# Optimization experiments

Measured on AMD Instinct MI355X. Metric: run time of the kernel, lower is better.

## Reference

```python
import jax, jax.numpy as jnp
import numpy as np

N = 8192
D_IN = 512
HID = 1024
EMB = 64
N_EFF = 2
N_CLASSES = 16
MARGIN = 0.01


def setup_inputs() -> dict:
    key = jax.random.key(0)
    ks = jax.random.split(key, 10)
    data = jax.random.normal(ks[0], (N, D_IN), dtype=jnp.float32)
    labels = jax.random.randint(ks[1], (N,), 0, N_CLASSES).astype(jnp.float32)
    x = jnp.concatenate([labels[:, None], data], axis=1)  # [N, 1+D_IN]

    def lin(k, fan_in, fan_out):
        return jax.random.normal(k, (fan_in, fan_out), dtype=jnp.float32) / np.sqrt(fan_in)

    return {
        "x": x,
        "W1": lin(ks[2], D_IN, HID), "b1": jnp.zeros((HID,), jnp.float32),
        "W2": lin(ks[3], HID, EMB), "b2": jnp.zeros((EMB,), jnp.float32),
        "W3": lin(ks[4], EMB, HID), "b3": jnp.zeros((HID,), jnp.float32),
        "W4": lin(ks[5], HID, D_IN), "b4": jnp.zeros((D_IN,), jnp.float32),
    }


def reference(x, W1, b1, W2, b2, W3, b3, W4, b4):
    labels = x[:, 0]
    data = x[:, 1:]

    # encoder / decoder (tanh MLP autoencoder)
    embedding = jnp.tanh(data @ W1 + b1) @ W2 + b2          # [N, EMB]
    decoded = jnp.tanh(embedding @ W3 + b3) @ W4 + b4       # [N, D_IN]

    conserved = embedding[:, N_EFF:]                        # [N, C]
    n_conserved = conserved.shape[1]

    # labels.expand + unique(return_inverse) on row-replicated labels is
    # equivalent to comparing the labels directly.
    lbl = labels.astype(jnp.int32)
    Y = lbl[:, None] != lbl[None, :]                        # [N, N] bool

    # D_mean[i,j] = mean_d (c_i - c_j)^2, via Gram-matrix algebra (one pass,
    # no [N,N,C] intermediate).
    sq = jnp.sum(conserved * conserved, axis=1)             # [N]
    gram = conserved @ conserved.T                          # [N, N]
    D_mean = jnp.maximum(sq[:, None] + sq[None, :] - 2.0 * gram, 0.0) / n_conserved

    Yf = Y.astype(D_mean.dtype)
    n_diff = jnp.sum(Yf)
    C_sim = jnp.sum(Yf * D_mean) / (n_diff + 1.0)
    C_diff = jnp.sum((1.0 - Yf) * jnp.maximum(0.0, MARGIN - D_mean)) / (
        (D_mean.shape[0] * D_mean.shape[1] - n_diff) + 1.0)

    return decoded, C_sim, C_diff
```

## Files before the change

### kernel.cpp

```cpp
#include <hip/hip_runtime.h>
#include <stdint.h>

#define NROWS 8192
#define DIN   512
#define HIDN  1024
#define EMBN  64
#define NCONS 62
#define NCLS  16
#define MARGINF 0.01f

typedef unsigned short u16;
typedef __attribute__((ext_vector_type(8))) short short8;
typedef __attribute__((ext_vector_type(4))) float floatx4;

__device__ __forceinline__ u16 f32_to_bf16(float f) {
  union { float f; uint32_t u; } x; x.f = f;
  uint32_t u = x.u;
  uint32_t r = (u + 0x7FFFu + ((u >> 16) & 1u)) >> 16;
  return (u16)r;
}

__device__ __forceinline__ float bf16_to_f32(u16 h) {
  union { uint32_t u; float f; } x; x.u = (uint32_t)h << 16;
  return x.f;
}

__device__ __forceinline__ float fast_tanh(float x) {
  float xc = fminf(fmaxf(x, -10.f), 10.f);
  float e = __expf(2.f * xc);
  return (e - 1.f) * __builtin_amdgcn_rcpf(e + 1.f);
}

__device__ __forceinline__ void load_lds16(const u16* g, u16* l) {
  __builtin_amdgcn_global_load_lds(
      (const __attribute__((address_space(1))) void*)g,
      (__attribute__((address_space(3))) void*)l, 16, 0, 0);
}

__device__ __forceinline__ void pack_tile(const float* __restrict__ W,
                                          u16* __restrict__ Wp,
                                          int N, int KU, int t, int lane)
{
  const int r = lane >> 2, slot = lane & 3;
  const int c = slot ^ ((r >> 1) & 3);
  const int nt = t / KU, ku = t - nt * KU;
  const int n = nt * 16 + r;
  const int kb = ku * 32 + c * 8;
  short8 v;
#pragma unroll
  for (int j = 0; j < 8; ++j) v[j] = (short)f32_to_bf16(W[(size_t)(kb + j) * N + n]);
  *(short8*)(Wp + ((size_t)t * 64 + lane) * 8) = v;
}

__global__ __launch_bounds__(256)
void prep_all(const float* __restrict__ x,
              const float* __restrict__ W1, const float* __restrict__ W2,
              const float* __restrict__ W3, const float* __restrict__ W4,
              u16* __restrict__ A0p, u16* __restrict__ W1p,
              u16* __restrict__ W2p, u16* __restrict__ W3p,
              u16* __restrict__ W4p, float* __restrict__ slab,
              int* __restrict__ labels, int* __restrict__ hist32)
{
  __shared__ int hh[NCLS];
  const int b = blockIdx.x;
  const int tid = threadIdx.x;
  const int tl = tid >> 6, lane = tid & 63;
  if (b < 2048) {
    if (b < 32) {
      if (tid < NCLS) hh[tid] = 0;
      const int row = b * 256 + tid;
      const int lab = (int)x[(size_t)row * 513];
      labels[row] = lab;
      __syncthreads();
      atomicAdd(&hh[lab], 1);
      __syncthreads();
      if (tid < NCLS) hist32[b * NCLS + tid] = hh[tid];
    }
    const int t = b * 4 + tl;
    const int rt = t >> 4, ku = t & 15;
    const int r = lane & 15, q = lane >> 4;
    const float* src = x + (size_t)(rt * 16 + r) * 513 + 1 + ku * 32 + q * 8;
    short8 v;
#pragma unroll
    for (int j = 0; j < 8; ++j) v[j] = (short)f32_to_bf16(src[j]);
    *(short8*)(A0p + ((size_t)t * 64 + lane) * 8) = v;
  } else if (b < 2304) {
    pack_tile(W1, W1p, 1024, 16, (b - 2048) * 4 + tl, lane);
  } else if (b < 2336) {
    pack_tile(W2, W2p, 64, 32, (b - 2304) * 4 + tl, lane);
  } else if (b < 2368) {
    pack_tile(W3, W3p, 1024, 2, (b - 2336) * 4 + tl, lane);
  } else if (b < 2624) {
    pack_tile(W4, W4p, 512, 32, (b - 2368) * 4 + tl, lane);
  } else {
    for (int i = tid; i < 4096; i += 256) slab[i] = 0.f;
  }
}

__global__ __launch_bounds__(256)
void gemm12(const u16* __restrict__ A0p, const u16* __restrict__ W1p,
            const float* __restrict__ b1, const u16* __restrict__ W2p,
            float* __restrict__ Ef4,
            const int* __restrict__ labels, const int* __restrict__ hist32,
            int* __restrict__ offs, int* __restrict__ counts,
            int* __restrict__ idx)
{
  __shared__ u16 lB[2][16 * 512];
  __shared__ u16 Hc[4][64 * 66];
  __shared__ int colsum[NCLS], preblk[NCLS], scur[NCLS];

  const int tid = threadIdx.x, wave = tid >> 6, lane = tid & 63;

  if (blockIdx.x >= 128) {
    const int sb = (blockIdx.x - 128) * 4 + blockIdx.y;
    if (tid < NCLS) {
      int s = 0, p = 0;
      for (int b2 = 0; b2 < 32; ++b2) {
        const int h = hist32[b2 * NCLS + tid];
        s += h;
        if (b2 < sb * 2) p += h;
      }
      colsum[tid] = s;
      preblk[tid] = p;
    }
    __syncthreads();
    if (tid < NCLS) {
      int o = 0;
      for (int c = 0; c < tid; ++c) o += colsum[c];
      scur[tid] = o + preblk[tid];
      if (sb == 0) {
        counts[tid] = colsum[tid];
        offs[tid] = o;
        if (tid == NCLS - 1) offs[NCLS] = o + colsum[NCLS - 1];
      }
    }
    __syncthreads();
    for (int i = tid; i < 512; i += 256) {
      const int row = sb * 512 + i;
      const int p = atomicAdd(&scur[labels[row]], 1);
      idx[p] = row;
    }
    return;
  }

  const int quad = lane >> 4, l15 = lane & 15;
  const int wm = wave >> 1, wn = wave & 1;
  const int xslot = (l15 >> 1) & 3;
  const int m0 = blockIdx.x * 64;
  const int g = blockIdx.y;

  floatx4 Hacc[4][2][2];
#pragma unroll
  for (int c = 0; c < 4; ++c)
#pragma unroll
    for (int i = 0; i < 2; ++i)
#pragma unroll
      for (int j = 0; j < 2; ++j) Hacc[c][i][j] = (floatx4){0.f, 0.f, 0.f, 0.f};

#pragma unroll
  for (int u = 0; u < 4; ++u) {
    const int jt = wave + u * 4;
    load_lds16(W1p + (size_t)((g * 16 + jt) * 16) * 512 + lane * 8, lB[0] + jt * 512);
  }
  __syncthreads();

  for (int s = 0; s < 16; ++s) {
    const int p = s & 1;
    if (s < 15) {
#pragma unroll
      for (int u = 0; u < 4; ++u) {
        const int jt = wave + u * 4;
        load_lds16(W1p + (size_t)((g * 16 + jt) * 16 + s + 1) * 512 + lane * 8,
                   lB[1 - p] + jt * 512);
      }
    }
    short8 af[2];
#pragma unroll
    for (int i = 0; i < 2; ++i)
      af[i] = *(const short8*)(A0p +
               (size_t)((blockIdx.x * 4 + wm * 2 + i) * 16 + s) * 512 + lane * 8);
#pragma unroll
    for (int c = 0; c < 4; ++c)
#pragma unroll
      for (int j = 0; j < 2; ++j) {
        const short8 bf = *(const short8*)(lB[p] + (c * 4 + wn * 2 + j) * 512
                              + l15 * 32 + ((quad ^ xslot) << 3));
#pragma unroll
        for (int i = 0; i < 2; ++i)
          Hacc[c][i][j] = __builtin_amdgcn_mfma_f32_16x16x32_bf16(af[i], bf, Hacc[c][i][j], 0, 0, 0);
      }
    __syncthreads();
  }

  u16* lW2 = &lB[0][0];
#pragma unroll
  for (int u = 0; u < 8; ++u) {
    const int t = wave * 8 + u;
    load_lds16(W2p + (size_t)((t >> 3) * 32 + g * 8 + (t & 7)) * 512 + lane * 8,
               lW2 + t * 512);
  }
#pragma unroll
  for (int c = 0; c < 4; ++c)
#pragma unroll
    for (int j = 0; j < 2; ++j) {
      const int col = wn * 32 + j * 16 + l15;
      const float bv = b1[g * 256 + c * 64 + col];
#pragma unroll
      for (int i = 0; i < 2; ++i)
#pragma unroll
        for (int r = 0; r < 4; ++r)
          Hc[c][(wm * 32 + i * 16 + quad * 4 + r) * 66 + col] =
              f32_to_bf16(fast_tanh(Hacc[c][i][j][r] + bv));
    }
  __syncthreads();

  floatx4 Eacc[2][2];
#pragma unroll
  for (int i = 0; i < 2; ++i)
#pragma unroll
    for (int j = 0; j < 2; ++j) Eacc[i][j] = (floatx4){0.f, 0.f, 0.f, 0.f};

#pragma unroll
  for (int es = 0; es < 8; ++es) {
    const int cc = es >> 1, hh2 = es & 1;
    short8 af2[2];
#pragma unroll
    for (int i = 0; i < 2; ++i)
      af2[i] = *(const short8*)(Hc[cc] + (wm * 32 + i * 16 + l15) * 66 + hh2 * 32 + quad * 8);
#pragma unroll
    for (int j = 0; j < 2; ++j) {
      const short8 bf = *(const short8*)(lW2 + ((wn * 2 + j) * 8 + es) * 512
                            + l15 * 32 + ((quad ^ xslot) << 3));
#pragma unroll
      for (int i = 0; i < 2; ++i)
        Eacc[i][j] = __builtin_amdgcn_mfma_f32_16x16x32_bf16(af2[i], bf, Eacc[i][j], 0, 0, 0);
    }
  }

  float* Efg = Ef4 + (size_t)g * NROWS * 64;
#pragma unroll
  for (int i = 0; i < 2; ++i)
#pragma unroll
    for (int j = 0; j < 2; ++j) {
      const int col = wn * 32 + j * 16 + l15;
#pragma unroll
      for (int r = 0; r < 4; ++r) {
        const int row = m0 + wm * 32 + i * 16 + quad * 4 + r;
        Efg[(size_t)row * 64 + col] = Eacc[i][j][r];
      }
    }
}

__global__ __launch_bounds__(256)
void gemm3(const u16* __restrict__ Ebf, const u16* __restrict__ W3p,
           const float* __restrict__ b3, u16* __restrict__ T)
{
  const int tid = threadIdx.x, wave = tid >> 6, lane = tid & 63;
  const int quad = lane >> 4, l15 = lane & 15;
  const int wm = wave >> 1, wn = wave & 1;
  const int c0 = blockIdx.x * 256;
  const int m0 = blockIdx.y * 64;
  const int lamb = l15 * 4 + (quad ^ ((l15 >> 1) & 3));

  floatx4 acc[2][8];
#pragma unroll
  for (int i = 0; i < 2; ++i)
#pragma unroll
    for (int jj = 0; jj < 8; ++jj) acc[i][jj] = (floatx4){0.f, 0.f, 0.f, 0.f};

#pragma unroll
  for (int kk = 0; kk < 2; ++kk) {
    short8 af[2];
#pragma unroll
    for (int i = 0; i < 2; ++i)
      af[i] = *(const short8*)(Ebf + (size_t)(m0 + wm * 32 + i * 16 + l15) * 64
                                   + kk * 32 + quad * 8);
#pragma unroll
    for (int jj = 0; jj < 8; ++jj) {
      const int nt = (c0 >> 4) + wn * 8 + jj;
      const short8 bf = *(const short8*)(W3p + (size_t)(nt * 2 + kk) * 512 + lamb * 8);
#pragma unroll
      for (int i = 0; i < 2; ++i)
        acc[i][jj] = __builtin_amdgcn_mfma_f32_16x16x32_bf16(af[i], bf, acc[i][jj], 0, 0, 0);
    }
  }

#pragma unroll
  for (int i = 0; i < 2; ++i)
#pragma unroll
    for (int jj = 0; jj < 8; ++jj) {
      const int col = c0 + wn * 128 + jj * 16 + l15;
      const float bv = b3[col];
#pragma unroll
      for (int r = 0; r < 4; ++r) {
        const int row = m0 + wm * 32 + i * 16 + quad * 4 + r;
        T[(size_t)row * 1024 + col] = f32_to_bf16(fast_tanh(acc[i][jj][r] + bv));
      }
    }
}

__global__ __launch_bounds__(256)
void gemm4(const u16* __restrict__ T, const u16* __restrict__ W4p,
           const float* __restrict__ b4, float* __restrict__ out)
{
  __shared__ u16 lA[2][16 * 512];
  __shared__ u16 lB[2][8 * 512];

  const int tid = threadIdx.x, wave = tid >> 6, lane = tid & 63;
  const int quad = lane >> 4, l15 = lane & 15;
  const int wm = wave >> 1, wn = wave & 1;
  const int xslot = (l15 >> 1) & 3;
  const int m0 = blockIdx.y * 128;
  const int n0 = blockIdx.x * 64;
  const int srow = lane >> 2;
  const int schunk = (lane & 3) ^ ((lane >> 3) & 3);

  auto stage = [&](int s, int buf) {
#pragma unroll
    for (int q = 0; q < 6; ++q) {
      const int u = wave + q * 4;
      if (u < 16) {
        const int rg = u >> 1, kh = u & 1;
        load_lds16(T + (size_t)(m0 + rg * 16 + srow) * 1024 + s * 64 + kh * 32 + schunk * 8,
                   (buf ? lA[1] : lA[0]) + u * 512 + lane * 8);
      } else {
        const int v = u - 16, nt = v >> 1, kh = v & 1;
        load_lds16(W4p + (size_t)(((n0 >> 4) + nt) * 32 + s * 2 + kh) * 512 + lane * 8,
                   (buf ? lB[1] : lB[0]) + v * 512 + lane * 8);
      }
    }
  };

  stage(0, 0);
  __syncthreads();

  floatx4 acc[4][2];
#pragma unroll
  for (int i = 0; i < 4; ++i)
#pragma unroll
    for (int j = 0; j < 2; ++j) acc[i][j] = (floatx4){0.f, 0.f, 0.f, 0.f};

  for (int s = 0; s < 16; ++s) {
    const int p = s & 1;
    if (s < 15) stage(s + 1, 1 - p);
#pragma unroll
    for (int kk = 0; kk < 2; ++kk) {
      short8 af[4], bf[2];
#pragma unroll
      for (int i = 0; i < 4; ++i)
        af[i] = *(const short8*)(lA[p] + ((wm * 4 + i) * 2 + kk) * 512
                                 + l15 * 32 + ((quad ^ xslot) << 3));
#pragma unroll
      for (int j = 0; j < 2; ++j)
        bf[j] = *(const short8*)(lB[p] + ((wn * 2 + j) * 2 + kk) * 512
                                 + l15 * 32 + ((quad ^ xslot) << 3));
#pragma unroll
      for (int i = 0; i < 4; ++i)
#pragma unroll
        for (int j = 0; j < 2; ++j)
          acc[i][j] = __builtin_amdgcn_mfma_f32_16x16x32_bf16(af[i], bf[j], acc[i][j], 0, 0, 0);
    }
    __syncthreads();
  }

#pragma unroll
  for (int i = 0; i < 4; ++i)
#pragma unroll
    for (int j = 0; j < 2; ++j) {
      const int col = n0 + wn * 32 + j * 16 + l15;
      const float bv = b4[col];
#pragma unroll
      for (int r = 0; r < 4; ++r) {
        const int row = m0 + wm * 64 + i * 16 + quad * 4 + r;
        out[(size_t)row * 512 + col] = acc[i][j][r] + bv;
      }
    }
}

__global__ __launch_bounds__(256)
void stats_sq(const float* __restrict__ Ef4, const float* __restrict__ b2,
              const int* __restrict__ labels, u16* __restrict__ Ebf,
              float* __restrict__ sqrow, float* __restrict__ vsum,
              float* __restrict__ Ssum)
{
  __shared__ float lv[NCLS][64];
  __shared__ float lsq[NCLS][64];
  const int tid = threadIdx.x;
  for (int i = tid; i < NCLS * 64; i += 256) {
    ((float*)lv)[i] = 0.f; ((float*)lsq)[i] = 0.f;
  }
  __syncthreads();

  const int wave = tid >> 6, lane = tid & 63;
  const float bv = b2[lane];
  const int base = blockIdx.x * 32 + wave * 8;
  for (int r = 0; r < 8; ++r) {
    const int row = base + r;
    const int c = labels[row];
    float acc = bv;
#pragma unroll
    for (int g = 0; g < 4; ++g)
      acc += Ef4[((size_t)g * NROWS + row) * 64 + lane];
    const u16 h = f32_to_bf16(acc);
    Ebf[(size_t)row * 64 + lane] = h;
    float v = bf16_to_f32(h);
    if (lane < 2) v = 0.f;
    const float v2 = v * v;
    atomicAdd(&lv[c][lane], v);
    atomicAdd(&lsq[c][lane], v2);
    float s = v2;
    for (int o = 32; o > 0; o >>= 1) s += __shfl_xor(s, o);
    if (lane == 0) sqrow[row] = s;
  }
  __syncthreads();

  for (int i = tid; i < NCLS * 64; i += 256) {
    const int c = i >> 6, k = i & 63;
    if (k >= 2) atomicAdd(&vsum[c * NCONS + k - 2], lv[c][k]);
  }
  if (tid < NCLS) {
    float s = 0.f;
    for (int k = 0; k < 64; ++k) s += lsq[tid][k];
    atomicAdd(&Ssum[tid], s);
  }
}

__global__ __launch_bounds__(256)
void pairwise_mfma(const u16* __restrict__ Ebf, const float* __restrict__ sqrow,
                   const int* __restrict__ idx, const int* __restrict__ offs,
                   float* __restrict__ pair_sum)
{
  const int cls = blockIdx.y;
  int p = blockIdx.x, ti = 0, cnt = 6;
  while (p >= cnt) { p -= cnt; ++ti; --cnt; }
  const int tj = ti + p;

  const int start = offs[cls];
  const int n = offs[cls + 1] - start;
  if (ti * 128 >= n || tj * 128 >= n) return;

  constexpr int LDA = 66;
  __shared__ u16 Li[128 * LDA];
  __shared__ u16 Lj[128 * LDA];
  __shared__ float sqI[128], sqJ[128];
  __shared__ float red4[4];

  const int tid = threadIdx.x;
  for (int e = tid; e < 2048; e += 256) {
    const int t = e >> 10;
    const int row = (e >> 3) & 127;
    const int ch = e & 7;
    const int g = (t ? tj : ti) * 128 + row;
    short8 v = (short8)0;
    if (g < n) {
      v = *(const short8*)(Ebf + (size_t)idx[start + g] * EMBN + ch * 8);
      if (ch == 0) { v[0] = 0; v[1] = 0; }
    }
    *(short8*)((t ? Lj : Li) + row * LDA + ch * 8) = v;
  }
  {
    const int t = tid >> 7, row = tid & 127;
    const int g = (t ? tj : ti) * 128 + row;
    (t ? sqJ : sqI)[row] = (g < n) ? sqrow[idx[start + g]] : 0.f;
  }
  __syncthreads();

  const int wave = tid >> 6, lane = tid & 63;
  const int wm = wave >> 1, wn = wave & 1;
  const int quad = lane >> 4, l15 = lane & 15;

  floatx4 acc[4][4];
#pragma unroll
  for (int i = 0; i < 4; ++i)
#pragma unroll
    for (int j = 0; j < 4; ++j) acc[i][j] = (floatx4){0.f, 0.f, 0.f, 0.f};

#pragma unroll
  for (int ks = 0; ks < 2; ++ks) {
    short8 af[4], bf[4];
#pragma unroll
    for (int i = 0; i < 4; ++i)
      af[i] = *(const short8*)(Li + (wm * 64 + i * 16 + l15) * LDA + ks * 32 + quad * 8);
#pragma unroll
    for (int j = 0; j < 4; ++j)
      bf[j] = *(const short8*)(Lj + (wn * 64 + j * 16 + l15) * LDA + ks * 32 + quad * 8);
#pragma unroll
    for (int i = 0; i < 4; ++i)
#pragma unroll
      for (int j = 0; j < 4; ++j)
        acc[i][j] = __builtin_amdgcn_mfma_f32_16x16x32_bf16(af[i], bf[j], acc[i][j], 0, 0, 0);
  }

  float local = 0.f;
#pragma unroll
  for (int i = 0; i < 4; ++i)
#pragma unroll
    for (int j = 0; j < 4; ++j)
#pragma unroll
      for (int r = 0; r < 4; ++r) {
        const int row = wm * 64 + i * 16 + quad * 4 + r;
        const int col = wn * 64 + j * 16 + l15;
        const int gi = ti * 128 + row, gj = tj * 128 + col;
        if (gi < n && gj < n && gi != gj) {
          const float D = (sqI[row] + sqJ[col] - 2.f * acc[i][j][r]) * (1.f / 62.f);
          local += fmaxf(0.f, MARGINF - D);
        }
      }
  if (ti < tj) local *= 2.f;

  for (int o = 32; o > 0; o >>= 1) local += __shfl_xor(local, o);
  if (lane == 0) red4[wave] = local;
  __syncthreads();
  if (tid == 0)
    atomicAdd(pair_sum, red4[0] + red4[1] + red4[2] + red4[3]);
}

__device__ __forceinline__ double block_reduce_d(double v, double* red, int tid) {
  red[tid] = v;
  __syncthreads();
  for (int st = 128; st > 0; st >>= 1) {
    if (tid < st) red[tid] += red[tid + st];
    __syncthreads();
  }
  const double r = red[0];
  __syncthreads();
  return r;
}

__global__ __launch_bounds__(256)
void finalize(const float* __restrict__ vsum, const float* __restrict__ Ssum,
              const int* __restrict__ counts, const float* __restrict__ pair_sum,
              float* __restrict__ out2)
{
  const int tid = threadIdx.x;
  __shared__ double red[256];

  double v = 0.0;
  if (tid < NCLS) v = (double)Ssum[tid] * (double)(NROWS - counts[tid]);
  const double t1 = block_reduce_d(v, red, tid);

  v = 0.0;
  if (tid < NCLS) { const double nc = (double)counts[tid]; v = nc * nc; }
  const double n_same = block_reduce_d(v, red, tid);

  v = 0.0;
  for (int i = tid; i < NCLS * NCONS; i += 256) { const double w = vsum[i]; v += w * w; }
  const double t2 = block_reduce_d(v, red, tid);

  v = 0.0;
  if (tid < NCONS) {
    double Vk = 0.0;
    for (int c = 0; c < NCLS; ++c) Vk += (double)vsum[c * NCONS + tid];
    v = Vk * Vk;
  }
  const double t3 = block_reduce_d(v, red, tid);

  if (tid == 0) {
    const double n_diff = (double)NROWS * (double)NROWS - n_same;
    const double sim = 2.0 * t1 - 2.0 * (t3 - t2);
    const double C_sim = sim / 62.0 / (n_diff + 1.0);
    const double C_diff = ((double)pair_sum[0] + (double)NROWS * (double)MARGINF)
                          / (n_same + 1.0);
    out2[0] = (float)C_sim;
    out2[1] = (float)C_diff;
  }
}

extern "C" void kernel_launch(void* const* d_in, const int* in_sizes, int n_in,
                              void* d_out, int out_size, void* d_ws, size_t ws_size,
                              hipStream_t stream)
{
  const float* x  = (const float*)d_in[0];
  const float* W1 = (const float*)d_in[1];
  const float* b1 = (const float*)d_in[2];
  const float* W2 = (const float*)d_in[3];
  const float* b2 = (const float*)d_in[4];
  const float* W3 = (const float*)d_in[5];
  const float* b3 = (const float*)d_in[6];
  const float* W4 = (const float*)d_in[7];
  const float* b4 = (const float*)d_in[8];
  float* out = (float*)d_out;

  char* ws = (char*)d_ws;
  const size_t KB = 1024, MB = 1ull << 20;
  u16* A0p    = (u16*)(ws + 0);
  u16* W1p    = (u16*)(ws + 8 * MB);
  u16* W2p    = (u16*)(ws + 9 * MB);
  u16* W3p    = (u16*)(ws + 9 * MB + 128 * KB);
  u16* W4p    = (u16*)(ws + 9 * MB + 256 * KB);
  float* Ef4  = (float*)(ws + 10 * MB + 256 * KB);
  u16* Ebf    = (u16*)(ws + 18 * MB + 256 * KB);
  int* labels = (int*)(ws + 19 * MB + 256 * KB);
  int* idx    = (int*)(ws + 19 * MB + 288 * KB);
  float* slab = (float*)(ws + 19 * MB + 320 * KB);
  int*   counts  = (int*)slab;
  int*   offs    = counts + 16;
  float* Ssum    = (float*)(counts + 96);
  float* psum    = (float*)(counts + 128);
  float* vsum    = (float*)(counts + 256);
  float* sqrow = (float*)(ws + 19 * MB + 336 * KB);
  int* hist32 = (int*)(ws + 19 * MB + 368 * KB);
  u16* T      = (u16*)(ws + 20 * MB);
  (void)in_sizes; (void)n_in; (void)out_size; (void)ws_size;

  prep_all<<<dim3(2625), dim3(256), 0, stream>>>(x, W1, W2, W3, W4,
                                                 A0p, W1p, W2p, W3p, W4p,
                                                 slab, labels, hist32);
  gemm12<<<dim3(132, 4), dim3(256), 0, stream>>>(A0p, W1p, b1, W2p, Ef4,
                                                 labels, hist32, offs, counts, idx);
  stats_sq<<<dim3(256), dim3(256), 0, stream>>>(Ef4, b2, labels, Ebf, sqrow, vsum, Ssum);
  gemm3<<<dim3(4, 128), dim3(256), 0, stream>>>(Ebf, W3p, b3, T);
  gemm4<<<dim3(8, 64), dim3(256), 0, stream>>>(T, W4p, b4, out);
  pairwise_mfma<<<dim3(21, 16), dim3(256), 0, stream>>>(Ebf, sqrow, idx, offs, psum);
  finalize<<<dim3(1), dim3(256), 0, stream>>>(vsum, Ssum, counts, psum,
                                              out + (size_t)NROWS * DIN);
}
```

Measured before the change: 180.0 us.

## Fuse embedding stats reduction with gemm3 and remap gemm4 block order

```diff
diff --git a/kernel.cpp b/kernel.cpp
--- a/kernel.cpp
+++ b/kernel.cpp
@@ -252,49 +252,93 @@
 }
 
 __global__ __launch_bounds__(256)
-void gemm3(const u16* __restrict__ Ebf, const u16* __restrict__ W3p,
-           const float* __restrict__ b3, u16* __restrict__ T)
-{
-  const int tid = threadIdx.x, wave = tid >> 6, lane = tid & 63;
+void stats3(const float* __restrict__ Ef4, const float* __restrict__ b2,
+            const int* __restrict__ labels, const u16* __restrict__ W3p,
+            const float* __restrict__ b3,
+            u16* __restrict__ Ebf, float* __restrict__ sqrow,
+            float* __restrict__ vsum, float* __restrict__ Ssum,
+            u16* __restrict__ T)
+{
+  __shared__ float lv[NCLS][64];
+  __shared__ float lsq[NCLS][64];
+  __shared__ u16 El[32 * 66];
+  const int tid = threadIdx.x;
+  for (int i = tid; i < NCLS * 64; i += 256) {
+    ((float*)lv)[i] = 0.f; ((float*)lsq)[i] = 0.f;
+  }
+  __syncthreads();
+
+  const int wave = tid >> 6, lane = tid & 63;
+  const float bv = b2[lane];
+  const int base0 = blockIdx.x * 32;
+  const int base = base0 + wave * 8;
+  for (int r = 0; r < 8; ++r) {
+    const int row = base + r;
+    const int c = labels[row];
+    float acc = bv;
+#pragma unroll
+    for (int g = 0; g < 4; ++g)
+      acc += Ef4[((size_t)g * NROWS + row) * 64 + lane];
+    const u16 h = f32_to_bf16(acc);
+    Ebf[(size_t)row * 64 + lane] = h;
+    El[(wave * 8 + r) * 66 + lane] = h;
+    float v = bf16_to_f32(h);
+    if (lane < 2) v = 0.f;
+    const float v2 = v * v;
+    atomicAdd(&lv[c][lane], v);
+    atomicAdd(&lsq[c][lane], v2);
+    float s = v2;
+    for (int o = 32; o > 0; o >>= 1) s += __shfl_xor(s, o);
+    if (lane == 0) sqrow[row] = s;
+  }
+  __syncthreads();
+
+  for (int i = tid; i < NCLS * 64; i += 256) {
+    const int c = i >> 6, k = i & 63;
+    if (k >= 2) atomicAdd(&vsum[c * NCONS + k - 2], lv[c][k]);
+  }
+  if (tid < NCLS) {
+    float s = 0.f;
+    for (int k = 0; k < 64; ++k) s += lsq[tid][k];
+    atomicAdd(&Ssum[tid], s);
+  }
+
   const int quad = lane >> 4, l15 = lane & 15;
-  const int wm = wave >> 1, wn = wave & 1;
-  const int c0 = blockIdx.x * 256;
-  const int m0 = blockIdx.y * 64;
+  const int wn = wave;
   const int lamb = l15 * 4 + (quad ^ ((l15 >> 1) & 3));
 
-  floatx4 acc[2][8];
+  floatx4 acc3[2][16];
 #pragma unroll
   for (int i = 0; i < 2; ++i)
 #pragma unroll
-    for (int jj = 0; jj < 8; ++jj) acc[i][jj] = (floatx4){0.f, 0.f, 0.f, 0.f};
+    for (int jj = 0; jj < 16; ++jj) acc3[i][jj] = (floatx4){0.f, 0.f, 0.f, 0.f};
 
 #pragma unroll
   for (int kk = 0; kk < 2; ++kk) {
     short8 af[2];
 #pragma unroll
     for (int i = 0; i < 2; ++i)
-      af[i] = *(const short8*)(Ebf + (size_t)(m0 + wm * 32 + i * 16 + l15) * 64
-                                   + kk * 32 + quad * 8);
-#pragma unroll
-    for (int jj = 0; jj < 8; ++jj) {
-      const int nt = (c0 >> 4) + wn * 8 + jj;
+      af[i] = *(const short8*)(El + (i * 16 + l15) * 66 + kk * 32 + quad * 8);
+#pragma unroll
+    for (int jj = 0; jj < 16; ++jj) {
+      const int nt = wn * 16 + jj;
       const short8 bf = *(const short8*)(W3p + (size_t)(nt * 2 + kk) * 512 + lamb * 8);
 #pragma unroll
       for (int i = 0; i < 2; ++i)
-        acc[i][jj] = __builtin_amdgcn_mfma_f32_16x16x32_bf16(af[i], bf, acc[i][jj], 0, 0, 0);
+        acc3[i][jj] = __builtin_amdgcn_mfma_f32_16x16x32_bf16(af[i], bf, acc3[i][jj], 0, 0, 0);
     }
   }
 
 #pragma unroll
   for (int i = 0; i < 2; ++i)
 #pragma unroll
-    for (int jj = 0; jj < 8; ++jj) {
-      const int col = c0 + wn * 128 + jj * 16 + l15;
-      const float bv = b3[col];
+    for (int jj = 0; jj < 16; ++jj) {
+      const int col = wn * 256 + jj * 16 + l15;
+      const float bv3 = b3[col];
 #pragma unroll
       for (int r = 0; r < 4; ++r) {
-        const int row = m0 + wm * 32 + i * 16 + quad * 4 + r;
-        T[(size_t)row * 1024 + col] = f32_to_bf16(fast_tanh(acc[i][jj][r] + bv));
+        const int row = base0 + i * 16 + quad * 4 + r;
+        T[(size_t)row * 1024 + col] = f32_to_bf16(fast_tanh(acc3[i][jj][r] + bv3));
       }
     }
 }
@@ -310,8 +354,9 @@
   const int quad = lane >> 4, l15 = lane & 15;
   const int wm = wave >> 1, wn = wave & 1;
   const int xslot = (l15 >> 1) & 3;
-  const int m0 = blockIdx.y * 128;
-  const int n0 = blockIdx.x * 64;
+  const int lin = blockIdx.x + (int)gridDim.x * blockIdx.y;
+  const int n0 = (lin >> 6) * 64;
+  const int m0 = (lin & 63) * 128;
   const int srow = lane >> 2;
   const int schunk = (lane & 3) ^ ((lane >> 3) & 3);
 
@@ -375,54 +420,6 @@
         out[(size_t)row * 512 + col] = acc[i][j][r] + bv;
       }
     }
-}
-
-__global__ __launch_bounds__(256)
-void stats_sq(const float* __restrict__ Ef4, const float* __restrict__ b2,
-              const int* __restrict__ labels, u16* __restrict__ Ebf,
-              float* __restrict__ sqrow, float* __restrict__ vsum,
-              float* __restrict__ Ssum)
-{
-  __shared__ float lv[NCLS][64];
-  __shared__ float lsq[NCLS][64];
-  const int tid = threadIdx.x;
-  for (int i = tid; i < NCLS * 64; i += 256) {
-    ((float*)lv)[i] = 0.f; ((float*)lsq)[i] = 0.f;
-  }
-  __syncthreads();
-
-  const int wave = tid >> 6, lane = tid & 63;
-  const float bv = b2[lane];
-  const int base = blockIdx.x * 32 + wave * 8;
-  for (int r = 0; r < 8; ++r) {
-    const int row = base + r;
-    const int c = labels[row];
-    float acc = bv;
-#pragma unroll
-    for (int g = 0; g < 4; ++g)
-      acc += Ef4[((size_t)g * NROWS + row) * 64 + lane];
-    const u16 h = f32_to_bf16(acc);
-    Ebf[(size_t)row * 64 + lane] = h;
-    float v = bf16_to_f32(h);
-    if (lane < 2) v = 0.f;
-    const float v2 = v * v;
-    atomicAdd(&lv[c][lane], v);
-    atomicAdd(&lsq[c][lane], v2);
-    float s = v2;
-    for (int o = 32; o > 0; o >>= 1) s += __shfl_xor(s, o);
-    if (lane == 0) sqrow[row] = s;
-  }
-  __syncthreads();
-
-  for (int i = tid; i < NCLS * 64; i += 256) {
-    const int c = i >> 6, k = i & 63;
-    if (k >= 2) atomicAdd(&vsum[c * NCONS + k - 2], lv[c][k]);
-  }
-  if (tid < NCLS) {
-    float s = 0.f;
-    for (int k = 0; k < 64; ++k) s += lsq[tid][k];
-    atomicAdd(&Ssum[tid], s);
-  }
 }
 
 __global__ __launch_bounds__(256)
@@ -608,8 +605,8 @@
                                                  slab, labels, hist32);
   gemm12<<<dim3(132, 4), dim3(256), 0, stream>>>(A0p, W1p, b1, W2p, Ef4,
                                                  labels, hist32, offs, counts, idx);
-  stats_sq<<<dim3(256), dim3(256), 0, stream>>>(Ef4, b2, labels, Ebf, sqrow, vsum, Ssum);
-  gemm3<<<dim3(4, 128), dim3(256), 0, stream>>>(Ebf, W3p, b3, T);
+  stats3<<<dim3(256), dim3(256), 0, stream>>>(Ef4, b2, labels, W3p, b3,
+                                              Ebf, sqrow, vsum, Ssum, T);
   gemm4<<<dim3(8, 64), dim3(256), 0, stream>>>(T, W4p, b4, out);
   pairwise_mfma<<<dim3(21, 16), dim3(256), 0, stream>>>(Ebf, sqrow, idx, offs, psum);
   finalize<<<dim3(1), dim3(256), 0, stream>>>(vsum, Ssum, counts, psum,
```

New measurement: 174.7 us. 2.9% less time.
